# Kernel optimization log

Hardware: AMD Instinct MI355X
Metric: run time of the kernel (lower is better)

The kernel has to match this reference:

```python
import jax, jax.numpy as jnp
import numpy as np

N_NODES = 100000
N_EDGES = 1600000


def setup_inputs() -> dict:
    key = jax.random.key(0)
    k1, k2, k3, k4, k5, k6 = jax.random.split(key, 6)
    x = jax.random.normal(k1, (N_NODES, 2), dtype=jnp.float32)
    edge_index = jax.random.randint(k2, (2, N_EDGES), 0, N_NODES, dtype=jnp.int64)
    # Glorot-style init for GCN weights, zeros for biases (PyG defaults)
    W1 = jax.random.normal(k3, (2, 64), dtype=jnp.float32) * (1.0 / np.sqrt(2.0))
    b1 = jnp.zeros((64,), dtype=jnp.float32)
    W2 = jax.random.normal(k4, (64, 1), dtype=jnp.float32) * (1.0 / np.sqrt(64.0))
    b2 = jnp.zeros((1,), dtype=jnp.float32)
    return {"x": x, "edge_index": edge_index, "W1": W1, "b1": b1, "W2": W2, "b2": b2}


def reference(x, edge_index, W1, b1, W2, b2):
    N = x.shape[0]
    row, col = edge_index[0], edge_index[1]  # source, target (PyG flow source_to_target)
    # symmetric GCN normalization, degrees from target index (no self loops)
    deg = jax.ops.segment_sum(jnp.ones(edge_index.shape[1], x.dtype), col, num_segments=N)
    deg_inv_sqrt = jnp.where(deg > 0, jnp.where(deg > 0, deg, 1.0) ** -0.5, 0.0)
    norm = (deg_inv_sqrt[row] * deg_inv_sqrt[col])[:, None]  # [E,1]

    def gcn_conv(h, W, b):
        h = h @ W                       # [N,F_out] tiny GEMM
        msg = h[row] * norm             # gather + scale: [E,F_out]
        agg = jax.ops.segment_sum(msg, col, num_segments=N)  # scatter-add
        return agg + b

    h = jax.nn.relu(gcn_conv(x, W1, b1))   # dropout is identity in eval mode
    out = jax.nn.relu(gcn_conv(h, W2, b2))
    return out
```

## Files before the change

### kernel.cpp

```cpp
#include <hip/hip_runtime.h>
#include <math.h>

#define NN 100000
#define NE 1600000
#define BKT 448
#define NB 224
#define EPB 6400
#define NPB 250
#define STRIDE 8192
#define RT 1024

__global__ void __launch_bounds__(RT) reorder_kernel(
        const int* __restrict__ row, const int* __restrict__ col,
        unsigned* __restrict__ cursor, unsigned* __restrict__ packed) {
    __shared__ int h[NB], lb[NB];
    __shared__ unsigned gaddr[NB], glim[NB];
    __shared__ int wsum[RT / 64];
    __shared__ uint2 sga[EPB];
    const int t = threadIdx.x;
    const int lane = t & 63, wid = t >> 6;
    const int e0 = blockIdx.x * EPB;

    for (int i = t; i < NB; i += RT) h[i] = 0;
    __syncthreads();

    const int4* rv = (const int4*)(row + e0);
    const int4* cv = (const int4*)(col + e0);
    unsigned pk[8]; int bb[8];
#pragma unroll
    for (int u = 0; u < 8; ++u) bb[u] = -1;
#pragma unroll
    for (int g = 0; g < 2; ++g) {
        int grp = g * RT + t;
        if (grp < EPB / 4) {
            int4 r4 = rv[grp], c4 = cv[grp];
            int rr[4] = {r4.x, r4.y, r4.z, r4.w};
            int cc[4] = {c4.x, c4.y, c4.z, c4.w};
#pragma unroll
            for (int j = 0; j < 4; ++j) {
                int b = cc[j] / BKT;
                int cl = cc[j] - b * BKT;
                pk[4 * g + j] = ((unsigned)rr[j] << 9) | (unsigned)cl;
                bb[4 * g + j] = b;
            }
        }
    }
#pragma unroll
    for (int u = 0; u < 8; ++u)
        if (bb[u] >= 0) atomicAdd(&h[bb[u]], 1);
    __syncthreads();

    int v = (t < NB) ? h[t] : 0;
    int incl = v;
#pragma unroll
    for (int d = 1; d < 64; d <<= 1) {
        int u2 = __shfl_up(incl, d);
        if (lane >= d) incl += u2;
    }
    if (lane == 63) wsum[wid] = incl;
    __syncthreads();
    int off = 0;
#pragma unroll
    for (int j = 0; j < 3; ++j)
        if (j < wid) off += wsum[j];
    if (t < NB) {
        lb[t] = off + incl - v;
        unsigned base = v ? atomicAdd(&cursor[t], (unsigned)v) : 0u;
        gaddr[t] = (unsigned)t * STRIDE + base;
        glim[t]  = (unsigned)(t + 1) * STRIDE;
    }
    __syncthreads();
    for (int i = t; i < NB; i += RT) h[i] = 0;
    __syncthreads();

#pragma unroll
    for (int u = 0; u < 8; ++u) {
        if (bb[u] >= 0) {
            int b = bb[u];
            int r = atomicAdd(&h[b], 1);
            unsigned a = gaddr[b] + (unsigned)r;
            if (a >= glim[b]) a = 0xFFFFFFFFu;
            sga[lb[b] + r] = make_uint2(pk[u], a);
        }
    }
    __syncthreads();
    for (int i = t; i < EPB; i += RT) {
        uint2 e = sga[i];
        if (e.y != 0xFFFFFFFFu) packed[e.y] = e.x;
    }
}

__global__ void __launch_bounds__(RT) degree_kernel(
        const unsigned* __restrict__ packed, const unsigned* __restrict__ cursor,
        const float2* __restrict__ x2,
        float* __restrict__ dis, float2* __restrict__ y2) {
    __shared__ int cnt[BKT];
    const int t = threadIdx.x;
    const int b = blockIdx.x;
    const unsigned s0 = (unsigned)b * STRIDE;
    const int L = min((int)cursor[b], STRIDE);
    const int L4 = L >> 2;

    for (int i = t; i < BKT; i += RT) cnt[i] = 0;
    __syncthreads();

    const uint4* pv4 = (const uint4*)(packed + s0);
    for (int g = t; g < L4; g += RT) {
        uint4 p4 = pv4[g];
        atomicAdd(&cnt[p4.x & 511u], 1);
        atomicAdd(&cnt[p4.y & 511u], 1);
        atomicAdd(&cnt[p4.z & 511u], 1);
        atomicAdd(&cnt[p4.w & 511u], 1);
    }
    for (int i = 4 * L4 + t; i < L; i += RT)
        atomicAdd(&cnt[packed[s0 + i] & 511u], 1);
    __syncthreads();

    int node = b * BKT + t;
    if (t < BKT && node < NN) {
        int v = cnt[t];
        float dv = (v > 0) ? rsqrtf((float)v) : 0.0f;
        dis[node] = dv;
        float2 xv = x2[node];
        y2[node] = make_float2(xv.x * dv, xv.y * dv);
    }
}

__global__ void __launch_bounds__(RT) conv1_kernel(
        const unsigned* __restrict__ packed, const unsigned* __restrict__ cursor,
        const float2* __restrict__ y2, const float* __restrict__ dis,
        const float* __restrict__ W1, const float* __restrict__ b1,
        const float* __restrict__ W2, float* __restrict__ z2) {
    __shared__ float accx[BKT], accy[BKT];
    __shared__ float sW0[64], sW1[64], sb1[64], sW2[64];
    const int t = threadIdx.x;
    const int b = blockIdx.x;
    const unsigned s0 = (unsigned)b * STRIDE;
    const int L = min((int)cursor[b], STRIDE);
    const int L4 = L >> 2;

    if (t < 64) { sW0[t] = W1[t]; sW1[t] = W1[64 + t]; sb1[t] = b1[t]; sW2[t] = W2[t]; }
    for (int i = t; i < BKT; i += RT) { accx[i] = 0.0f; accy[i] = 0.0f; }
    __syncthreads();

    const uint4* pv4 = (const uint4*)(packed + s0);
    for (int g = t; g < L4; g += RT) {
        uint4 p4 = pv4[g];
        unsigned pp[4] = {p4.x, p4.y, p4.z, p4.w};
        float2 vv[4];
#pragma unroll
        for (int j = 0; j < 4; ++j) vv[j] = y2[pp[j] >> 9];
#pragma unroll
        for (int j = 0; j < 4; ++j) {
            int cl = pp[j] & 511u;
            atomicAdd(&accx[cl], vv[j].x);
            atomicAdd(&accy[cl], vv[j].y);
        }
    }
    for (int i = 4 * L4 + t; i < L; i += RT) {
        unsigned p = packed[s0 + i];
        float2 v = y2[p >> 9];
        int cl = p & 511u;
        atomicAdd(&accx[cl], v.x);
        atomicAdd(&accy[cl], v.y);
    }
    __syncthreads();

    int node = b * BKT + t;
    if (t < BKT && node < NN) {
        float dv = dis[node];
        float a0 = accx[t] * dv, a1 = accy[t] * dv;
        float acc = 0.0f;
#pragma unroll
        for (int j = 0; j < 64; ++j) {
            float h = fmaf(a0, sW0[j], fmaf(a1, sW1[j], sb1[j]));
            acc = fmaf(fmaxf(h, 0.0f), sW2[j], acc);
        }
        z2[node] = acc * dv;
    }
}

__global__ void __launch_bounds__(RT) conv2_kernel(
        const unsigned* __restrict__ packed, const unsigned* __restrict__ cursor,
        const float* __restrict__ z2, const float* __restrict__ dis,
        const float* __restrict__ b2, float* __restrict__ out) {
    __shared__ float acc[BKT];
    const int t = threadIdx.x;
    const int b = blockIdx.x;
    const unsigned s0 = (unsigned)b * STRIDE;
    const int L = min((int)cursor[b], STRIDE);
    const int L4 = L >> 2;

    for (int i = t; i < BKT; i += RT) acc[i] = 0.0f;
    __syncthreads();

    const uint4* pv4 = (const uint4*)(packed + s0);
    for (int g = t; g < L4; g += RT) {
        uint4 p4 = pv4[g];
        unsigned pp[4] = {p4.x, p4.y, p4.z, p4.w};
        float vv[4];
#pragma unroll
        for (int j = 0; j < 4; ++j) vv[j] = z2[pp[j] >> 9];
#pragma unroll
        for (int j = 0; j < 4; ++j)
            atomicAdd(&acc[pp[j] & 511u], vv[j]);
    }
    for (int i = 4 * L4 + t; i < L; i += RT) {
        unsigned p = packed[s0 + i];
        atomicAdd(&acc[p & 511u], z2[p >> 9]);
    }
    __syncthreads();

    int node = b * BKT + t;
    if (t < BKT && node < NN)
        out[node] = fmaxf(fmaf(dis[node], acc[t], b2[0]), 0.0f);
}

extern "C" void kernel_launch(void* const* d_in, const int* in_sizes, int n_in,
                              void* d_out, int out_size, void* d_ws, size_t ws_size,
                              hipStream_t stream) {
    const float* x  = (const float*)d_in[0];
    const int*   ei = (const int*)d_in[1];
    const float* W1 = (const float*)d_in[2];
    const float* b1 = (const float*)d_in[3];
    const float* W2 = (const float*)d_in[4];
    const float* b2 = (const float*)d_in[5];
    float* out = (float*)d_out;

    const int* row = ei;
    const int* col = ei + NE;

    unsigned* packed   = (unsigned*)d_ws;
    float2*   y2       = (float2*)(packed + (size_t)NB * STRIDE);
    float*    dis      = (float*)(y2 + NN);
    float*    z2       = dis + NN;
    unsigned* cursor   = (unsigned*)(z2 + NN);

    hipMemsetAsync(cursor, 0, NB * sizeof(unsigned), stream);

    reorder_kernel<<<NPB, RT, 0, stream>>>(row, col, cursor, packed);
    degree_kernel <<<NB, RT, 0, stream>>>(packed, cursor, (const float2*)x, dis, y2);
    conv1_kernel  <<<NB, RT, 0, stream>>>(packed, cursor, y2, dis, W1, b1, W2, z2);
    conv2_kernel  <<<NB, RT, 0, stream>>>(packed, cursor, z2, dis, b2, out);
}
```

Measured before the change: 120.1 us.

## Replace bucketed LDS scatter with direct global atomic edge aggregation

Drops the edge reordering into per-bucket packed lists and the shared-memory accumulation. Degree counts and both GCN aggregations are now done with edge-parallel global atomics, plus separate node-wise kernels for the MLP and the output. This removes the reorder pass and its scratch traffic, but adds many contended random global atomics and extra reads of the edge index arrays.

```diff
diff --git a/kernel.cpp b/kernel.cpp
--- a/kernel.cpp
+++ b/kernel.cpp
@@ -3,217 +3,88 @@
 
 #define NN 100000
 #define NE 1600000
-#define BKT 448
-#define NB 224
-#define EPB 6400
-#define NPB 250
-#define STRIDE 8192
-#define RT 1024
+#define NG (NE / 4)
 
-__global__ void __launch_bounds__(RT) reorder_kernel(
+__global__ void __launch_bounds__(256) deg_kernel(
+        const int* __restrict__ col, unsigned* __restrict__ deg) {
+    int g = blockIdx.x * 256 + threadIdx.x;
+    if (g >= NG) return;
+    int4 c4 = ((const int4*)col)[g];
+    atomicAdd(&deg[c4.x], 1u);
+    atomicAdd(&deg[c4.y], 1u);
+    atomicAdd(&deg[c4.z], 1u);
+    atomicAdd(&deg[c4.w], 1u);
+}
+
+__global__ void __launch_bounds__(256) conv1_agg_kernel(
         const int* __restrict__ row, const int* __restrict__ col,
-        unsigned* __restrict__ cursor, unsigned* __restrict__ packed) {
-    __shared__ int h[NB], lb[NB];
-    __shared__ unsigned gaddr[NB], glim[NB];
-    __shared__ int wsum[RT / 64];
-    __shared__ uint2 sga[EPB];
-    const int t = threadIdx.x;
-    const int lane = t & 63, wid = t >> 6;
-    const int e0 = blockIdx.x * EPB;
-
-    for (int i = t; i < NB; i += RT) h[i] = 0;
-    __syncthreads();
-
-    const int4* rv = (const int4*)(row + e0);
-    const int4* cv = (const int4*)(col + e0);
-    unsigned pk[8]; int bb[8];
+        const float2* __restrict__ x2, const unsigned* __restrict__ deg,
+        float2* __restrict__ agg1) {
+    int g = blockIdx.x * 256 + threadIdx.x;
+    if (g >= NG) return;
+    int4 r4 = ((const int4*)row)[g];
+    int4 c4 = ((const int4*)col)[g];
+    int rr[4] = {r4.x, r4.y, r4.z, r4.w};
+    int cc[4] = {c4.x, c4.y, c4.z, c4.w};
+    float2 xv[4]; unsigned dg[4];
 #pragma unroll
-    for (int u = 0; u < 8; ++u) bb[u] = -1;
-#pragma unroll
-    for (int g = 0; g < 2; ++g) {
-        int grp = g * RT + t;
-        if (grp < EPB / 4) {
-            int4 r4 = rv[grp], c4 = cv[grp];
-            int rr[4] = {r4.x, r4.y, r4.z, r4.w};
-            int cc[4] = {c4.x, c4.y, c4.z, c4.w};
-#pragma unroll
-            for (int j = 0; j < 4; ++j) {
-                int b = cc[j] / BKT;
-                int cl = cc[j] - b * BKT;
-                pk[4 * g + j] = ((unsigned)rr[j] << 9) | (unsigned)cl;
-                bb[4 * g + j] = b;
-            }
-        }
+    for (int j = 0; j < 4; ++j) {
+        xv[j] = x2[rr[j]];
+        dg[j] = deg[rr[j]];
     }
 #pragma unroll
-    for (int u = 0; u < 8; ++u)
-        if (bb[u] >= 0) atomicAdd(&h[bb[u]], 1);
-    __syncthreads();
-
-    int v = (t < NB) ? h[t] : 0;
-    int incl = v;
-#pragma unroll
-    for (int d = 1; d < 64; d <<= 1) {
-        int u2 = __shfl_up(incl, d);
-        if (lane >= d) incl += u2;
-    }
-    if (lane == 63) wsum[wid] = incl;
-    __syncthreads();
-    int off = 0;
-#pragma unroll
-    for (int j = 0; j < 3; ++j)
-        if (j < wid) off += wsum[j];
-    if (t < NB) {
-        lb[t] = off + incl - v;
-        unsigned base = v ? atomicAdd(&cursor[t], (unsigned)v) : 0u;
-        gaddr[t] = (unsigned)t * STRIDE + base;
-        glim[t]  = (unsigned)(t + 1) * STRIDE;
-    }
-    __syncthreads();
-    for (int i = t; i < NB; i += RT) h[i] = 0;
-    __syncthreads();
-
-#pragma unroll
-    for (int u = 0; u < 8; ++u) {
-        if (bb[u] >= 0) {
-            int b = bb[u];
-            int r = atomicAdd(&h[b], 1);
-            unsigned a = gaddr[b] + (unsigned)r;
-            if (a >= glim[b]) a = 0xFFFFFFFFu;
-            sga[lb[b] + r] = make_uint2(pk[u], a);
-        }
-    }
-    __syncthreads();
-    for (int i = t; i < EPB; i += RT) {
-        uint2 e = sga[i];
-        if (e.y != 0xFFFFFFFFu) packed[e.y] = e.x;
+    for (int j = 0; j < 4; ++j) {
+        float dv = dg[j] ? rsqrtf((float)dg[j]) : 0.0f;
+        atomicAdd(&agg1[cc[j]].x, xv[j].x * dv);
+        atomicAdd(&agg1[cc[j]].y, xv[j].y * dv);
     }
 }
 
-__global__ void __launch_bounds__(RT) degree_kernel(
-        const unsigned* __restrict__ packed, const unsigned* __restrict__ cursor,
-        const float2* __restrict__ x2,
-        float* __restrict__ dis, float2* __restrict__ y2) {
-    __shared__ int cnt[BKT];
-    const int t = threadIdx.x;
-    const int b = blockIdx.x;
-    const unsigned s0 = (unsigned)b * STRIDE;
-    const int L = min((int)cursor[b], STRIDE);
-    const int L4 = L >> 2;
-
-    for (int i = t; i < BKT; i += RT) cnt[i] = 0;
+__global__ void __launch_bounds__(256) mlp_kernel(
+        const float2* __restrict__ agg1, const unsigned* __restrict__ deg,
+        const float* __restrict__ W1, const float* __restrict__ b1,
+        const float* __restrict__ W2, float* __restrict__ z2) {
+    __shared__ float sW0[64], sW1[64], sb1[64], sW2[64];
+    int t = threadIdx.x;
+    if (t < 64) { sW0[t] = W1[t]; sW1[t] = W1[64 + t]; sb1[t] = b1[t]; sW2[t] = W2[t]; }
     __syncthreads();
-
-    const uint4* pv4 = (const uint4*)(packed + s0);
-    for (int g = t; g < L4; g += RT) {
-        uint4 p4 = pv4[g];
-        atomicAdd(&cnt[p4.x & 511u], 1);
-        atomicAdd(&cnt[p4.y & 511u], 1);
-        atomicAdd(&cnt[p4.z & 511u], 1);
-        atomicAdd(&cnt[p4.w & 511u], 1);
+    int n = blockIdx.x * 256 + t;
+    if (n >= NN) return;
+    unsigned d = deg[n];
+    float dv = d ? rsqrtf((float)d) : 0.0f;
+    float2 a = agg1[n];
+    float a0 = a.x * dv, a1 = a.y * dv;
+    float acc = 0.0f;
+#pragma unroll
+    for (int j = 0; j < 64; ++j) {
+        float h = fmaf(a0, sW0[j], fmaf(a1, sW1[j], sb1[j]));
+        acc = fmaf(fmaxf(h, 0.0f), sW2[j], acc);
     }
-    for (int i = 4 * L4 + t; i < L; i += RT)
-        atomicAdd(&cnt[packed[s0 + i] & 511u], 1);
-    __syncthreads();
-
-    int node = b * BKT + t;
-    if (t < BKT && node < NN) {
-        int v = cnt[t];
-        float dv = (v > 0) ? rsqrtf((float)v) : 0.0f;
-        dis[node] = dv;
-        float2 xv = x2[node];
-        y2[node] = make_float2(xv.x * dv, xv.y * dv);
-    }
+    z2[n] = acc * dv;
 }
 
-__global__ void __launch_bounds__(RT) conv1_kernel(
-        const unsigned* __restrict__ packed, const unsigned* __restrict__ cursor,
-        const float2* __restrict__ y2, const float* __restrict__ dis,
-        const float* __restrict__ W1, const float* __restrict__ b1,
-        const float* __restrict__ W2, float* __restrict__ z2) {
-    __shared__ float accx[BKT], accy[BKT];
-    __shared__ float sW0[64], sW1[64], sb1[64], sW2[64];
-    const int t = threadIdx.x;
-    const int b = blockIdx.x;
-    const unsigned s0 = (unsigned)b * STRIDE;
-    const int L = min((int)cursor[b], STRIDE);
-    const int L4 = L >> 2;
-
-    if (t < 64) { sW0[t] = W1[t]; sW1[t] = W1[64 + t]; sb1[t] = b1[t]; sW2[t] = W2[t]; }
-    for (int i = t; i < BKT; i += RT) { accx[i] = 0.0f; accy[i] = 0.0f; }
-    __syncthreads();
-
-    const uint4* pv4 = (const uint4*)(packed + s0);
-    for (int g = t; g < L4; g += RT) {
-        uint4 p4 = pv4[g];
-        unsigned pp[4] = {p4.x, p4.y, p4.z, p4.w};
-        float2 vv[4];
-#pragma unroll
-        for (int j = 0; j < 4; ++j) vv[j] = y2[pp[j] >> 9];
-#pragma unroll
-        for (int j = 0; j < 4; ++j) {
-            int cl = pp[j] & 511u;
-            atomicAdd(&accx[cl], vv[j].x);
-            atomicAdd(&accy[cl], vv[j].y);
-        }
-    }
-    for (int i = 4 * L4 + t; i < L; i += RT) {
-        unsigned p = packed[s0 + i];
-        float2 v = y2[p >> 9];
-        int cl = p & 511u;
-        atomicAdd(&accx[cl], v.x);
-        atomicAdd(&accy[cl], v.y);
-    }
-    __syncthreads();
-
-    int node = b * BKT + t;
-    if (t < BKT && node < NN) {
-        float dv = dis[node];
-        float a0 = accx[t] * dv, a1 = accy[t] * dv;
-        float acc = 0.0f;
-#pragma unroll
-        for (int j = 0; j < 64; ++j) {
-            float h = fmaf(a0, sW0[j], fmaf(a1, sW1[j], sb1[j]));
-            acc = fmaf(fmaxf(h, 0.0f), sW2[j], acc);
-        }
-        z2[node] = acc * dv;
-    }
+__global__ void __launch_bounds__(256) conv2_agg_kernel(
+        const int* __restrict__ row, const int* __restrict__ col,
+        const float* __restrict__ z2, float* __restrict__ agg2) {
+    int g = blockIdx.x * 256 + threadIdx.x;
+    if (g >= NG) return;
+    int4 r4 = ((const int4*)row)[g];
+    int4 c4 = ((const int4*)col)[g];
+    float zv[4] = {z2[r4.x], z2[r4.y], z2[r4.z], z2[r4.w]};
+    atomicAdd(&agg2[c4.x], zv[0]);
+    atomicAdd(&agg2[c4.y], zv[1]);
+    atomicAdd(&agg2[c4.z], zv[2]);
+    atomicAdd(&agg2[c4.w], zv[3]);
 }
 
-__global__ void __launch_bounds__(RT) conv2_kernel(
-        const unsigned* __restrict__ packed, const unsigned* __restrict__ cursor,
-        const float* __restrict__ z2, const float* __restrict__ dis,
+__global__ void __launch_bounds__(256) out_kernel(
+        const float* __restrict__ agg2, const unsigned* __restrict__ deg,
         const float* __restrict__ b2, float* __restrict__ out) {
-    __shared__ float acc[BKT];
-    const int t = threadIdx.x;
-    const int b = blockIdx.x;
-    const unsigned s0 = (unsigned)b * STRIDE;
-    const int L = min((int)cursor[b], STRIDE);
-    const int L4 = L >> 2;
-
-    for (int i = t; i < BKT; i += RT) acc[i] = 0.0f;
-    __syncthreads();
-
-    const uint4* pv4 = (const uint4*)(packed + s0);
-    for (int g = t; g < L4; g += RT) {
-        uint4 p4 = pv4[g];
-        unsigned pp[4] = {p4.x, p4.y, p4.z, p4.w};
-        float vv[4];
-#pragma unroll
-        for (int j = 0; j < 4; ++j) vv[j] = z2[pp[j] >> 9];
-#pragma unroll
-        for (int j = 0; j < 4; ++j)
-            atomicAdd(&acc[pp[j] & 511u], vv[j]);
-    }
-    for (int i = 4 * L4 + t; i < L; i += RT) {
-        unsigned p = packed[s0 + i];
-        atomicAdd(&acc[p & 511u], z2[p >> 9]);
-    }
-    __syncthreads();
-
-    int node = b * BKT + t;
-    if (t < BKT && node < NN)
-        out[node] = fmaxf(fmaf(dis[node], acc[t], b2[0]), 0.0f);
+    int n = blockIdx.x * 256 + threadIdx.x;
+    if (n >= NN) return;
+    unsigned d = deg[n];
+    float dv = d ? rsqrtf((float)d) : 0.0f;
+    out[n] = fmaxf(fmaf(dv, agg2[n], b2[0]), 0.0f);
 }
 
 extern "C" void kernel_launch(void* const* d_in, const int* in_sizes, int n_in,
@@ -230,16 +101,18 @@
     const int* row = ei;
     const int* col = ei + NE;
 
-    unsigned* packed   = (unsigned*)d_ws;
-    float2*   y2       = (float2*)(packed + (size_t)NB * STRIDE);
-    float*    dis      = (float*)(y2 + NN);
-    float*    z2       = dis + NN;
-    unsigned* cursor   = (unsigned*)(z2 + NN);
+    unsigned* deg  = (unsigned*)d_ws;
+    float2*   agg1 = (float2*)(deg + NN);
+    float*    agg2 = (float*)(agg1 + NN);
+    float*    z2   = agg2 + NN;
 
-    hipMemsetAsync(cursor, 0, NB * sizeof(unsigned), stream);
+    hipMemsetAsync(deg, 0, (size_t)NN * (4 + 8 + 4), stream);
 
-    reorder_kernel<<<NPB, RT, 0, stream>>>(row, col, cursor, packed);
-    degree_kernel <<<NB, RT, 0, stream>>>(packed, cursor, (const float2*)x, dis, y2);
-    conv1_kernel  <<<NB, RT, 0, stream>>>(packed, cursor, y2, dis, W1, b1, W2, z2);
-    conv2_kernel  <<<NB, RT, 0, stream>>>(packed, cursor, z2, dis, b2, out);
+    const int gE = (NG + 255) / 256;
+    const int gN = (NN + 255) / 256;
+    deg_kernel      <<<gE, 256, 0, stream>>>(col, deg);
+    conv1_agg_kernel<<<gE, 256, 0, stream>>>(row, col, (const float2*)x, deg, agg1);
+    mlp_kernel      <<<gN, 256, 0, stream>>>(agg1, deg, W1, b1, W2, z2);
+    conv2_agg_kernel<<<gE, 256, 0, stream>>>(row, col, z2, agg2);
+    out_kernel      <<<gN, 256, 0, stream>>>(agg2, deg, b2, out);
 }
```

After: 392.2 us. 226% more time.
